# Optimization experiments

Measured on AMD Instinct MI355X. Metric: run time of the kernel, lower is better.

The kernel has to match this reference:

```python
import jax, jax.numpy as jnp
import numpy as np

BN_EPS = 1e-5
NUM_SUBSET = 3


def _conv1x1(x, W, b):
    # x: [B,C,T,J], W: [O,C], b: [O] -> [B,O,T,J]
    return jnp.einsum('bctj,oc->botj', x, W) + b[:, None, None]


def _bn_eval(y, gamma, beta, mean, var):
    inv = gamma / jnp.sqrt(var + BN_EPS)
    return y * inv[:, None, None] + (beta - mean * inv)[:, None, None]


def setup_inputs() -> dict:
    key = jax.random.key(0)
    ks = jax.random.split(key, 8)
    B, Cin, T, J = 64, 64, 300, 25
    Cout, inter = 128, 32
    s = 0.05
    return {
        'x': jax.random.normal(ks[0], (B, Cin, T, J), jnp.float32),
        'PA': jax.random.normal(ks[1], (NUM_SUBSET, J, J), jnp.float32) * s,
        'Wa': jax.random.normal(ks[2], (NUM_SUBSET, inter, Cin), jnp.float32) * s,
        'ba': jnp.zeros((NUM_SUBSET, inter), jnp.float32),
        'Wb': jax.random.normal(ks[3], (NUM_SUBSET, inter, Cin), jnp.float32) * s,
        'bb': jnp.zeros((NUM_SUBSET, inter), jnp.float32),
        'Wd': jax.random.normal(ks[4], (NUM_SUBSET, Cout, Cin), jnp.float32) * s,
        'bd': jnp.zeros((NUM_SUBSET, Cout), jnp.float32),
        'Wdown': jax.random.normal(ks[5], (Cout, Cin), jnp.float32) * s,
        'bdown': jnp.zeros((Cout,), jnp.float32),
        'bn_gamma': jnp.ones((Cout,), jnp.float32),
        'bn_beta': jnp.zeros((Cout,), jnp.float32),
        'bn_mean': jnp.zeros((Cout,), jnp.float32),
        'bn_var': jnp.ones((Cout,), jnp.float32),
        'down_gamma': jnp.ones((Cout,), jnp.float32),
        'down_beta': jnp.zeros((Cout,), jnp.float32),
        'down_mean': jnp.zeros((Cout,), jnp.float32),
        'down_var': jnp.ones((Cout,), jnp.float32),
    }


def reference(x, PA, Wa, ba, Wb, bb, Wd, bd, Wdown, bdown,
              bn_gamma, bn_beta, bn_mean, bn_var,
              down_gamma, down_beta, down_mean, down_var):
    B, C, T, J = x.shape
    A = PA + jnp.eye(J, dtype=x.dtype)  # [S,J,J]
    x_flat = x.reshape(B, C * T, J)
    y = None
    for i in range(NUM_SUBSET):
        # theta/phi embeddings via 1x1 convs -> [B,inter,T,J]
        A1 = _conv1x1(x, Wa[i], ba[i])
        A2 = _conv1x1(x, Wb[i], bb[i])
        A1 = A1.transpose(0, 3, 1, 2).reshape(B, J, -1)  # [B,J,inter*T]
        A2 = A2.reshape(B, -1, J)                          # [B,inter*T,J]
        scores = jnp.matmul(A1, A2) / A1.shape[-1]         # [B,J,J]
        Aadapt = jax.nn.softmax(scores, axis=-2) + A[i]    # softmax over dim -2
        z = jnp.matmul(x_flat, Aadapt).reshape(B, C, T, J)
        z = _conv1x1(z, Wd[i], bd[i])                      # [B,Cout,T,J]
        y = z if y is None else y + z
    y = _bn_eval(y, bn_gamma, bn_beta, bn_mean, bn_var)
    res = _bn_eval(_conv1x1(x, Wdown, bdown), down_gamma, down_beta, down_mean, down_var)
    return jax.nn.relu(y + res)
```

## Files before the change

### kernel.cpp

```cpp
#include <hip/hip_runtime.h>
#include <math.h>

#define T_DIM 300
#define J_DIM 25
#define CIN 64
#define COUT 128
#define B_DIM 64

typedef __attribute__((ext_vector_type(8))) short bf16x8;
typedef __attribute__((ext_vector_type(4))) float f32x4;

__device__ __forceinline__ unsigned short f2bf(float f) {
    union { float f; unsigned u; } v; v.f = f;
    unsigned r = v.u + 0x7FFF + ((v.u >> 16) & 1);
    return (unsigned short)(r >> 16);
}

__device__ __forceinline__ unsigned pkbf(float lo, float hi) {
    return (unsigned)f2bf(lo) | ((unsigned)f2bf(hi) << 16);
}

#define SC_NSEG 10
#define SC_NCH  3

__global__ __launch_bounds__(256, 2) void scores_kernel(
    const float* __restrict__ x,
    const uint4* __restrict__ Wf,
    const float* __restrict__ ba, const float* __restrict__ bb,
    float* __restrict__ part)
{
    __shared__ uint4 xsf[8][256];
    __shared__ unsigned short aT1[32][328];
    __shared__ unsigned short aT2[32][328];

    const int tid  = threadIdx.x;
    const int seg  = blockIdx.x;
    const int b    = blockIdx.y;
    const int lane = tid & 63;
    const int w    = tid >> 6;
    const int g4   = lane >> 4;
    const int c16  = lane & 15;
    const int jt1  = w >> 1, jt2 = w & 1;

    const float* xb = x + (size_t)b * (CIN * T_DIM * J_DIM);

    f32x4 gacc[3];
    #pragma unroll
    for (int i = 0; i < 3; ++i) gacc[i] = (f32x4){0.f, 0.f, 0.f, 0.f};

    for (int ch = 0; ch < SC_NCH; ++ch) {
        const int pb = seg * 750 + ch * 250;

        #pragma unroll
        for (int cg = 0; cg < 8; ++cg) {
            int p = pb + tid; if (p > 7499) p = 7499;
            const float* xc = xb + (size_t)(cg * 8) * 7500 + p;
            unsigned d[4];
            #pragma unroll
            for (int m = 0; m < 4; ++m)
                d[m] = (unsigned)f2bf(xc[(2 * m) * 7500]) |
                       ((unsigned)f2bf(xc[(2 * m + 1) * 7500]) << 16);
            xsf[cg][tid] = make_uint4(d[0], d[1], d[2], d[3]);
        }
        __syncthreads();

        #pragma unroll
        for (int i = 0; i < 3; ++i) {
            #pragma unroll
            for (int pass = 0; pass < 2; ++pass) {
                const float* bs = pass ? bb : ba;
                bf16x8 afr[2][2];
                #pragma unroll
                for (int m = 0; m < 2; ++m)
                    #pragma unroll
                    for (int s = 0; s < 2; ++s)
                        afr[m][s] = *reinterpret_cast<const bf16x8*>(
                            &Wf[((((i * 2 + pass) * 2 + m) * 2 + s) << 6) + lane]);
                f32x4 acc[2][4];
                #pragma unroll
                for (int m = 0; m < 2; ++m) {
                    float4 bv = *(const float4*)(bs + i * 32 + m * 16 + g4 * 4);
                    #pragma unroll
                    for (int n = 0; n < 4; ++n)
                        acc[m][n] = (f32x4){bv.x, bv.y, bv.z, bv.w};
                }
                #pragma unroll
                for (int n = 0; n < 4; ++n) {
                    const int ptile = w * 4 + n;
                    #pragma unroll
                    for (int s = 0; s < 2; ++s) {
                        bf16x8 bfr = *reinterpret_cast<const bf16x8*>(&xsf[s * 4 + g4][ptile * 16 + c16]);
                        #pragma unroll
                        for (int m = 0; m < 2; ++m)
                            acc[m][n] = __builtin_amdgcn_mfma_f32_16x16x32_bf16(
                                afr[m][s], bfr, acc[m][n], 0, 0, 0);
                    }
                }
                unsigned short (*aT)[328] = pass ? aT2 : aT1;
                #pragma unroll
                for (int n = 0; n < 4; ++n) {
                    const int pos = (w * 4 + n) * 16 + c16;
                    if (pos < 250) {
                        const int t = pos / 25, j = pos - t * 25;
                        #pragma unroll
                        for (int m = 0; m < 2; ++m) {
                            const int kbase = t * 32 + m * 16 + g4 * 4;
                            uint2 pk = make_uint2(pkbf(acc[m][n][0], acc[m][n][1]),
                                                  pkbf(acc[m][n][2], acc[m][n][3]));
                            *reinterpret_cast<uint2*>(&aT[j][kbase]) = pk;
                        }
                    }
                }
            }
            __syncthreads();

            #pragma unroll
            for (int s = 0; s < 10; ++s) {
                bf16x8 af = *reinterpret_cast<const bf16x8*>(&aT1[jt1 * 16 + c16][s * 32 + g4 * 8]);
                bf16x8 bf = *reinterpret_cast<const bf16x8*>(&aT2[jt2 * 16 + c16][s * 32 + g4 * 8]);
                gacc[i] = __builtin_amdgcn_mfma_f32_16x16x32_bf16(af, bf, gacc[i], 0, 0, 0);
            }
            __syncthreads();
        }
    }

    #pragma unroll
    for (int i = 0; i < 3; ++i) {
        const int j2 = jt2 * 16 + c16;
        #pragma unroll
        for (int r = 0; r < 4; ++r) {
            const int j1 = jt1 * 16 + g4 * 4 + r;
            if (j1 < 25 && j2 < 25)
                part[((size_t)(b * 3 + i) * SC_NSEG + seg) * 625 + j1 * 25 + j2] = gacc[i][r];
        }
    }
}

__global__ void softmax_kernel(const float* __restrict__ part,
                               const float* __restrict__ PA,
                               uint4* __restrict__ Gbg)
{
    int bi = blockIdx.x;
    int b = bi / 3, i = bi - b * 3;
    int j2 = threadIdx.x;
    if (j2 >= 32) return;
    float gval[25];
    if (j2 < 25) {
        float v[25];
        float m = -1e30f;
        #pragma unroll
        for (int j1 = 0; j1 < 25; ++j1) {
            float s = 0.0f;
            for (int seg = 0; seg < SC_NSEG; ++seg)
                s += part[((size_t)bi * SC_NSEG + seg) * 625 + j1 * 25 + j2];
            v[j1] = s * (1.0f / 9600.0f);
            m = fmaxf(m, v[j1]);
        }
        float sum = 0.0f;
        #pragma unroll
        for (int j1 = 0; j1 < 25; ++j1) { v[j1] = expf(v[j1] - m); sum += v[j1]; }
        float r = 1.0f / sum;
        #pragma unroll
        for (int j1 = 0; j1 < 25; ++j1)
            gval[j1] = v[j1] * r + PA[(i * 25 + j1) * 25 + j2] + (j1 == j2 ? 1.0f : 0.0f);
    }
    #pragma unroll
    for (int kg = 0; kg < 4; ++kg) {
        unsigned d[4];
        #pragma unroll
        for (int mm = 0; mm < 4; ++mm) {
            int ja = kg * 8 + 2 * mm, jb2 = ja + 1;
            float va = (j2 < 25 && ja < 25) ? gval[ja] : 0.0f;
            float vb = (j2 < 25 && jb2 < 25) ? gval[jb2] : 0.0f;
            d[mm] = pkbf(va, vb);
        }
        Gbg[((size_t)bi * 4 + kg) * 33 + j2] = make_uint4(d[0], d[1], d[2], d[3]);
    }
}

__global__ void prep_kernel(
    const float* __restrict__ Wd, const float* __restrict__ bd,
    const float* __restrict__ Wdown, const float* __restrict__ bdown,
    const float* __restrict__ g1, const float* __restrict__ b1,
    const float* __restrict__ m1, const float* __restrict__ v1,
    const float* __restrict__ g2, const float* __restrict__ b2,
    const float* __restrict__ m2, const float* __restrict__ v2,
    const float* __restrict__ Wa, const float* __restrict__ Wb,
    unsigned short* __restrict__ Wpb, float* __restrict__ cst,
    uint4* __restrict__ Wf)
{
    const int tid = threadIdx.x;
    for (int idx = tid; idx < COUT * 256; idx += 256) {
        int o = idx >> 8, k = idx & 255;
        int region = k >> 6;
        float val;
        if (region == 1) {
            float inv = g2[o] * rsqrtf(v2[o] + 1e-5f);
            val = Wdown[o * 64 + (k & 63)] * inv;
        } else {
            int i = (region == 0) ? 0 : region - 1;
            float inv = g1[o] * rsqrtf(v1[o] + 1e-5f);
            val = Wd[(i * COUT + o) * 64 + (k & 63)] * inv;
        }
        Wpb[idx] = f2bf(val);
    }
    for (int idx = tid; idx < 24 * 64; idx += 256) {
        const int fi = idx >> 6, lane = idx & 63;
        const int i = fi >> 3, pass = (fi >> 2) & 1, m = (fi >> 1) & 1, s = fi & 1;
        const int g4 = lane >> 4, c16 = lane & 15;
        const float* W = pass ? Wb : Wa;
        const float* wp = W + i * 2048 + (m * 16 + c16) * 64 + s * 32 + g4 * 8;
        Wf[idx] = make_uint4(pkbf(wp[0], wp[1]), pkbf(wp[2], wp[3]),
                             pkbf(wp[4], wp[5]), pkbf(wp[6], wp[7]));
    }
    if (tid < COUT) {
        int o = tid;
        float inv1 = g1[o] * rsqrtf(v1[o] + 1e-5f);
        float inv2 = g2[o] * rsqrtf(v2[o] + 1e-5f);
        cst[o] = (bd[o] + bd[COUT + o] + bd[2 * COUT + o]) * inv1
               + (b1[o] - m1[o] * inv1)
               + bdown[o] * inv2
               + (b2[o] - m2[o] * inv2);
    }
}

#define M_NCH 75

__global__ __launch_bounds__(512, 8) void main_kernel(
    const float* __restrict__ x, const uint4* __restrict__ Gbg,
    const unsigned short* __restrict__ Wpb, const float* __restrict__ cst,
    float* __restrict__ out)
{
    __shared__ uint4 zxs[16][113];
    __shared__ uint4 gb[396];

    const int tid  = threadIdx.x;
    const int b    = blockIdx.y;
    const int t0   = blockIdx.x * 4;
    const int lane = tid & 63;
    const int w    = __builtin_amdgcn_readfirstlane(tid >> 6);
    const int g4   = lane >> 4;
    const int c16  = lane & 15;

    const float* xb = x + (size_t)b * (CIN * T_DIM * J_DIM) + t0 * 25;

    #pragma unroll
    for (int it = 0; it < 4; ++it) {
        const int u = tid + it * 512;
        const int quad = u & 7, t = (u >> 3) & 3, c = u >> 5;
        const int jp0 = quad * 4;
        const int kg = 8 + (c >> 3);
        const int sl = c & 7;
        #pragma unroll
        for (int e = 0; e < 4; ++e) {
            const int jp = jp0 + e;
            if (jp < 25)
                *((unsigned short*)&zxs[kg][t * 25 + jp] + sl) = f2bf(xb[c * 7500 + t * 25 + jp]);
        }
    }
    if (tid < 396) gb[tid] = Gbg[(size_t)b * 396 + tid];

    f32x4 acc[7];
    #pragma unroll
    for (int n = 0; n < 7; ++n) acc[n] = (f32x4){0.f, 0.f, 0.f, 0.f};

    const int zt = w >> 1;
    const int mh = w & 1;

    __syncthreads();

    bf16x8 a_x[2];
    #pragma unroll
    for (int m = 0; m < 2; ++m) {
        const int cA = (mh * 2 + m) * 16 + c16;
        const unsigned short* src = (const unsigned short*)&zxs[8 + (cA >> 3)][zt * 25] + (cA & 7);
        bf16x8 t;
        #pragma unroll
        for (int e = 0; e < 8; ++e) {
            const int jp = g4 * 8 + e;
            t[e] = (jp < 25) ? (short)src[jp * 8] : (short)0;
        }
        a_x[m] = t;
    }

    auto zpass = [&](int i, int kb) {
        #pragma unroll
        for (int n = 0; n < 2; ++n) {
            bf16x8 bfr = *reinterpret_cast<const bf16x8*>(&gb[(i * 4 + g4) * 33 + n * 16 + c16]);
            #pragma unroll
            for (int m = 0; m < 2; ++m) {
                f32x4 d = __builtin_amdgcn_mfma_f32_16x16x32_bf16(
                    a_x[m], bfr, (f32x4){0.f, 0.f, 0.f, 0.f}, 0, 0, 0);
                const int j = n * 16 + c16;
                if (j < 25) {
                    const int cb = (mh * 2 + m) * 16 + g4 * 4;
                    const int kg = kb + (cb >> 3);
                    const int hf = (cb >> 2) & 1;
                    unsigned lo = pkbf(d[0], d[1]), hi = pkbf(d[2], d[3]);
                    *reinterpret_cast<uint2*>(
                        reinterpret_cast<char*>(&zxs[kg][zt * 25 + j]) + hf * 8) = make_uint2(lo, hi);
                }
            }
        }
    };

    zpass(0, 0);
    __syncthreads();

    {
        const unsigned short* wrow = Wpb + (w * 16 + c16) * 256 + g4 * 8;
        #pragma unroll
        for (int kk = 0; kk < 4; ++kk) {
            bf16x8 afr = *reinterpret_cast<const bf16x8*>(wrow + kk * 32);
            #pragma unroll
            for (int n = 0; n < 7; ++n) {
                bf16x8 bfr = *reinterpret_cast<const bf16x8*>(&zxs[kk * 4 + g4][n * 16 + c16]);
                acc[n] = __builtin_amdgcn_mfma_f32_16x16x32_bf16(afr, bfr, acc[n], 0, 0, 0);
            }
        }
    }
    __syncthreads();

    zpass(1, 0);
    zpass(2, 8);
    __syncthreads();

    {
        const unsigned short* wrow = Wpb + (w * 16 + c16) * 256 + 128 + g4 * 8;
        #pragma unroll
        for (int kk = 0; kk < 4; ++kk) {
            bf16x8 afr = *reinterpret_cast<const bf16x8*>(wrow + kk * 32);
            #pragma unroll
            for (int n = 0; n < 7; ++n) {
                bf16x8 bfr = *reinterpret_cast<const bf16x8*>(&zxs[kk * 4 + g4][n * 16 + c16]);
                acc[n] = __builtin_amdgcn_mfma_f32_16x16x32_bf16(afr, bfr, acc[n], 0, 0, 0);
            }
        }
    }

    float* ob = out + (size_t)b * (COUT * T_DIM * J_DIM) + t0 * 25;
    #pragma unroll
    for (int r = 0; r < 4; ++r) {
        const int o = w * 16 + g4 * 4 + r;
        const float cv = cst[o];
        #pragma unroll
        for (int n = 0; n < 7; ++n) {
            const int pos = n * 16 + c16;
            if (pos < 100)
                ob[(size_t)o * 7500 + pos] = fmaxf(acc[n][r] + cv, 0.0f);
        }
    }
}

extern "C" void kernel_launch(void* const* d_in, const int* in_sizes, int n_in,
                              void* d_out, int out_size, void* d_ws, size_t ws_size,
                              hipStream_t stream)
{
    const float* x     = (const float*)d_in[0];
    const float* PA    = (const float*)d_in[1];
    const float* Wa    = (const float*)d_in[2];
    const float* ba    = (const float*)d_in[3];
    const float* Wb    = (const float*)d_in[4];
    const float* bb    = (const float*)d_in[5];
    const float* Wd    = (const float*)d_in[6];
    const float* bd    = (const float*)d_in[7];
    const float* Wdown = (const float*)d_in[8];
    const float* bdown = (const float*)d_in[9];
    const float* bn_g  = (const float*)d_in[10];
    const float* bn_b  = (const float*)d_in[11];
    const float* bn_m  = (const float*)d_in[12];
    const float* bn_v  = (const float*)d_in[13];
    const float* dn_g  = (const float*)d_in[14];
    const float* dn_b  = (const float*)d_in[15];
    const float* dn_m  = (const float*)d_in[16];
    const float* dn_v  = (const float*)d_in[17];

    float* ws   = (float*)d_ws;
    float* part = ws;
    uint4* Gbg  = (uint4*)(ws + 1200000);
    float* cst  = ws + 1301376;
    unsigned short* Wpb = (unsigned short*)(ws + 1301504);
    uint4* Wf   = (uint4*)(ws + 1317888);

    prep_kernel<<<1, 256, 0, stream>>>(Wd, bd, Wdown, bdown,
        bn_g, bn_b, bn_m, bn_v, dn_g, dn_b, dn_m, dn_v, Wa, Wb, Wpb, cst, Wf);
    scores_kernel<<<dim3(SC_NSEG, B_DIM), 256, 0, stream>>>(x, Wf, ba, bb, part);
    softmax_kernel<<<dim3(B_DIM * 3), 64, 0, stream>>>(part, PA, Gbg);
    main_kernel<<<dim3(M_NCH, B_DIM), 512, 0, stream>>>(x, Gbg, Wpb, cst, (float*)d_out);
}
```

Baseline: 256.9 us.

## Merge the two output GEMM phases into one K=256 pass with a larger LDS buffer

The LDS staging buffer doubles so that all three z projections and x fit at once, and the two-phase output GEMM with its extra barriers becomes a single K=256 MFMA loop. Weight fragments are preloaded into registers before the x load, and x is loaded with float4 reads and packed two channels at a time. The weight packing order is changed to [Wd0,Wd1,Wd2,Wdown] to match. Launch bounds drop to 4 waves per SIMD because LDS and register use rise, which lowers occupancy.

Result: slower. 271.5 us (+5.7%).

```diff
diff --git a/kernel.cpp b/kernel.cpp
--- a/kernel.cpp
+++ b/kernel.cpp
@@ -194,13 +194,12 @@
         int o = idx >> 8, k = idx & 255;
         int region = k >> 6;
         float val;
-        if (region == 1) {
+        if (region == 3) {
             float inv = g2[o] * rsqrtf(v2[o] + 1e-5f);
             val = Wdown[o * 64 + (k & 63)] * inv;
         } else {
-            int i = (region == 0) ? 0 : region - 1;
             float inv = g1[o] * rsqrtf(v1[o] + 1e-5f);
-            val = Wd[(i * COUT + o) * 64 + (k & 63)] * inv;
+            val = Wd[(region * COUT + o) * 64 + (k & 63)] * inv;
         }
         Wpb[idx] = f2bf(val);
     }
@@ -226,12 +225,12 @@
 
 #define M_NCH 75
 
-__global__ __launch_bounds__(512, 8) void main_kernel(
+__global__ __launch_bounds__(512, 4) void main_kernel(
     const float* __restrict__ x, const uint4* __restrict__ Gbg,
     const unsigned short* __restrict__ Wpb, const float* __restrict__ cst,
     float* __restrict__ out)
 {
-    __shared__ uint4 zxs[16][113];
+    __shared__ uint4 zxs[32][113];
     __shared__ uint4 gb[396];
 
     const int tid  = threadIdx.x;
@@ -244,18 +243,34 @@
 
     const float* xb = x + (size_t)b * (CIN * T_DIM * J_DIM) + t0 * 25;
 
-    #pragma unroll
-    for (int it = 0; it < 4; ++it) {
-        const int u = tid + it * 512;
-        const int quad = u & 7, t = (u >> 3) & 3, c = u >> 5;
+    bf16x8 afr[8];
+    {
+        const unsigned short* wrow = Wpb + (w * 16 + c16) * 256 + g4 * 8;
+        #pragma unroll
+        for (int kk = 0; kk < 8; ++kk)
+            afr[kk] = *reinterpret_cast<const bf16x8*>(wrow + kk * 32);
+    }
+
+    #pragma unroll
+    for (int it = 0; it < 2; ++it) {
+        const int u   = tid + it * 512;
+        const int quad = u & 7, t = (u >> 3) & 3, c2 = u >> 5;
         const int jp0 = quad * 4;
-        const int kg = 8 + (c >> 3);
-        const int sl = c & 7;
-        #pragma unroll
-        for (int e = 0; e < 4; ++e) {
-            const int jp = jp0 + e;
-            if (jp < 25)
-                *((unsigned short*)&zxs[kg][t * 25 + jp] + sl) = f2bf(xb[c * 7500 + t * 25 + jp]);
+        const int kg  = 24 + (c2 >> 2);
+        const int sl2 = c2 & 3;
+        const float* base = xb + (2 * c2) * 7500 + t * 25 + jp0;
+        if (quad < 6) {
+            float4 va = *(const float4*)(base);
+            float4 vb = *(const float4*)(base + 7500);
+            #pragma unroll
+            for (int e = 0; e < 4; ++e) {
+                const int jp = jp0 + e;
+                ((unsigned*)&zxs[kg][t * 25 + jp])[sl2] =
+                    pkbf(((const float*)&va)[e], ((const float*)&vb)[e]);
+            }
+        } else if (quad == 6) {
+            float a = base[0], bvv = base[7500];
+            ((unsigned*)&zxs[kg][t * 25 + 24])[sl2] = pkbf(a, bvv);
         }
     }
     if (tid < 396) gb[tid] = Gbg[(size_t)b * 396 + tid];
@@ -273,7 +288,7 @@
     #pragma unroll
     for (int m = 0; m < 2; ++m) {
         const int cA = (mh * 2 + m) * 16 + c16;
-        const unsigned short* src = (const unsigned short*)&zxs[8 + (cA >> 3)][zt * 25] + (cA & 7);
+        const unsigned short* src = (const unsigned short*)&zxs[24 + (cA >> 3)][zt * 25] + (cA & 7);
         bf16x8 t;
         #pragma unroll
         for (int e = 0; e < 8; ++e) {
@@ -305,36 +320,16 @@
     };
 
     zpass(0, 0);
+    zpass(1, 8);
+    zpass(2, 16);
     __syncthreads();
 
-    {
-        const unsigned short* wrow = Wpb + (w * 16 + c16) * 256 + g4 * 8;
-        #pragma unroll
-        for (int kk = 0; kk < 4; ++kk) {
-            bf16x8 afr = *reinterpret_cast<const bf16x8*>(wrow + kk * 32);
-            #pragma unroll
-            for (int n = 0; n < 7; ++n) {
-                bf16x8 bfr = *reinterpret_cast<const bf16x8*>(&zxs[kk * 4 + g4][n * 16 + c16]);
-                acc[n] = __builtin_amdgcn_mfma_f32_16x16x32_bf16(afr, bfr, acc[n], 0, 0, 0);
-            }
-        }
-    }
-    __syncthreads();
-
-    zpass(1, 0);
-    zpass(2, 8);
-    __syncthreads();
-
-    {
-        const unsigned short* wrow = Wpb + (w * 16 + c16) * 256 + 128 + g4 * 8;
-        #pragma unroll
-        for (int kk = 0; kk < 4; ++kk) {
-            bf16x8 afr = *reinterpret_cast<const bf16x8*>(wrow + kk * 32);
-            #pragma unroll
-            for (int n = 0; n < 7; ++n) {
-                bf16x8 bfr = *reinterpret_cast<const bf16x8*>(&zxs[kk * 4 + g4][n * 16 + c16]);
-                acc[n] = __builtin_amdgcn_mfma_f32_16x16x32_bf16(afr, bfr, acc[n], 0, 0, 0);
-            }
+    #pragma unroll
+    for (int kk = 0; kk < 8; ++kk) {
+        #pragma unroll
+        for (int n = 0; n < 7; ++n) {
+            bf16x8 bfr = *reinterpret_cast<const bf16x8*>(&zxs[kk * 4 + g4][n * 16 + c16]);
+            acc[n] = __builtin_amdgcn_mfma_f32_16x16x32_bf16(afr[kk], bfr, acc[n], 0, 0, 0);
         }
     }
 
```

## Pre-pack x into channel-interleaved bf16 once and reuse in both kernels

Applied to the files above, without the earlier changes.

Adds an xpack kernel that converts x to bf16 and packs 8 channels per uint4 in workspace. The scores and main kernels then load these packed vectors directly instead of each converting fp32 scattered loads. This removes the duplicated conversion work and the strided gathers, but adds an extra kernel launch and a write plus re-read of the packed buffer.

After: 254.5 us. Within noise of the previous version (-0.9%).

```diff
diff --git a/kernel.cpp b/kernel.cpp
--- a/kernel.cpp
+++ b/kernel.cpp
@@ -20,11 +20,34 @@
     return (unsigned)f2bf(lo) | ((unsigned)f2bf(hi) << 16);
 }
 
+__global__ __launch_bounds__(256) void xpack_kernel(const float* __restrict__ x,
+                                                    uint4* __restrict__ xpk)
+{
+    __shared__ float xs[8][250];
+    const int tid = threadIdx.x;
+    const int p0  = blockIdx.x * 250;
+    const int cg  = blockIdx.y;
+    const int b   = blockIdx.z;
+    const float* xb = x + ((size_t)b * 64 + cg * 8) * 7500 + p0;
+    for (int idx = tid; idx < 2000; idx += 256) {
+        int c = idx / 250, pp = idx - c * 250;
+        xs[c][pp] = xb[c * 7500 + pp];
+    }
+    __syncthreads();
+    uint4* dst = xpk + ((size_t)b * 8 + cg) * 7500 + p0;
+    for (int pp = tid; pp < 250; pp += 256) {
+        dst[pp] = make_uint4(pkbf(xs[0][pp], xs[1][pp]),
+                             pkbf(xs[2][pp], xs[3][pp]),
+                             pkbf(xs[4][pp], xs[5][pp]),
+                             pkbf(xs[6][pp], xs[7][pp]));
+    }
+}
+
 #define SC_NSEG 10
 #define SC_NCH  3
 
 __global__ __launch_bounds__(256, 2) void scores_kernel(
-    const float* __restrict__ x,
+    const uint4* __restrict__ xpk,
     const uint4* __restrict__ Wf,
     const float* __restrict__ ba, const float* __restrict__ bb,
     float* __restrict__ part)
@@ -42,7 +65,7 @@
     const int c16  = lane & 15;
     const int jt1  = w >> 1, jt2 = w & 1;
 
-    const float* xb = x + (size_t)b * (CIN * T_DIM * J_DIM);
+    const uint4* xpb = xpk + (size_t)b * 8 * 7500;
 
     f32x4 gacc[3];
     #pragma unroll
@@ -51,16 +74,11 @@
     for (int ch = 0; ch < SC_NCH; ++ch) {
         const int pb = seg * 750 + ch * 250;
 
-        #pragma unroll
-        for (int cg = 0; cg < 8; ++cg) {
+        {
             int p = pb + tid; if (p > 7499) p = 7499;
-            const float* xc = xb + (size_t)(cg * 8) * 7500 + p;
-            unsigned d[4];
-            #pragma unroll
-            for (int m = 0; m < 4; ++m)
-                d[m] = (unsigned)f2bf(xc[(2 * m) * 7500]) |
-                       ((unsigned)f2bf(xc[(2 * m + 1) * 7500]) << 16);
-            xsf[cg][tid] = make_uint4(d[0], d[1], d[2], d[3]);
+            #pragma unroll
+            for (int cg = 0; cg < 8; ++cg)
+                xsf[cg][tid] = xpb[cg * 7500 + p];
         }
         __syncthreads();
 
@@ -227,7 +245,7 @@
 #define M_NCH 75
 
 __global__ __launch_bounds__(512, 8) void main_kernel(
-    const float* __restrict__ x, const uint4* __restrict__ Gbg,
+    const uint4* __restrict__ xpk, const uint4* __restrict__ Gbg,
     const unsigned short* __restrict__ Wpb, const float* __restrict__ cst,
     float* __restrict__ out)
 {
@@ -242,20 +260,11 @@
     const int g4   = lane >> 4;
     const int c16  = lane & 15;
 
-    const float* xb = x + (size_t)b * (CIN * T_DIM * J_DIM) + t0 * 25;
-
-    #pragma unroll
-    for (int it = 0; it < 4; ++it) {
-        const int u = tid + it * 512;
-        const int quad = u & 7, t = (u >> 3) & 3, c = u >> 5;
-        const int jp0 = quad * 4;
-        const int kg = 8 + (c >> 3);
-        const int sl = c & 7;
-        #pragma unroll
-        for (int e = 0; e < 4; ++e) {
-            const int jp = jp0 + e;
-            if (jp < 25)
-                *((unsigned short*)&zxs[kg][t * 25 + jp] + sl) = f2bf(xb[c * 7500 + t * 25 + jp]);
+    {
+        const uint4* xpb = xpk + (size_t)b * 8 * 7500 + t0 * 25;
+        for (int idx = tid; idx < 800; idx += 512) {
+            int kgl = idx / 100, q = idx - kgl * 100;
+            zxs[8 + kgl][q] = xpb[kgl * 7500 + q];
         }
     }
     if (tid < 396) gb[tid] = Gbg[(size_t)b * 396 + tid];
@@ -381,10 +390,12 @@
     float* cst  = ws + 1301376;
     unsigned short* Wpb = (unsigned short*)(ws + 1301504);
     uint4* Wf   = (uint4*)(ws + 1317888);
+    uint4* xpk  = (uint4*)(ws + 1324032);
 
     prep_kernel<<<1, 256, 0, stream>>>(Wd, bd, Wdown, bdown,
         bn_g, bn_b, bn_m, bn_v, dn_g, dn_b, dn_m, dn_v, Wa, Wb, Wpb, cst, Wf);
-    scores_kernel<<<dim3(SC_NSEG, B_DIM), 256, 0, stream>>>(x, Wf, ba, bb, part);
+    xpack_kernel<<<dim3(30, 8, B_DIM), 256, 0, stream>>>(x, xpk);
+    scores_kernel<<<dim3(SC_NSEG, B_DIM), 256, 0, stream>>>(xpk, Wf, ba, bb, part);
     softmax_kernel<<<dim3(B_DIM * 3), 64, 0, stream>>>(part, PA, Gbg);
-    main_kernel<<<dim3(M_NCH, B_DIM), 512, 0, stream>>>(x, Gbg, Wpb, cst, (float*)d_out);
-}
+    main_kernel<<<dim3(M_NCH, B_DIM), 512, 0, stream>>>(xpk, Gbg, Wpb, cst, (float*)d_out);
+}
```
